# Kernel tuning notes

Hardware: AMD Instinct MI355X
Metric: run time of the kernel (lower is better)

The kernel has to match this reference:

```python
import jax, jax.numpy as jnp
import numpy as np
from jax import lax

CAP = 15.0
EPS = 1e-6

def _rmsnorm(x, w):
    xf = x.astype(jnp.float32)
    var = jnp.mean(xf * xf, axis=-1, keepdims=True)
    return w * (xf * lax.rsqrt(var + EPS)).astype(x.dtype)

def _softcap_sigmoid(x):
    return jax.nn.sigmoid(CAP * jnp.tanh(x / CAP))

def setup_inputs() -> dict:
    key = jax.random.key(0)
    ks = jax.random.split(key, 4)
    B, S, D, P = 8, 2048, 1024, 1365
    x = jax.random.normal(ks[0], (B, S, D), dtype=jnp.float32)
    h0 = jnp.zeros((B, P), dtype=jnp.float32)
    ln_weight = jnp.ones((D,), dtype=jnp.float32)
    gate_w = jax.random.normal(ks[1], (3 * P, D), dtype=jnp.float32) * 0.02
    cell_w = jax.random.normal(ks[2], (P, D), dtype=jnp.float32) * 0.02
    out_w = jax.random.normal(ks[3], (D, P), dtype=jnp.float32) * 0.02
    return {"x": x, "h0": h0, "ln_weight": ln_weight, "gate_w": gate_w,
            "cell_w": cell_w, "out_w": out_w}

def reference(x, h0, ln_weight, gate_w, cell_w, out_w):
    B, S, D = x.shape
    P = cell_w.shape[0]
    residual = x
    xn = _rmsnorm(x, ln_weight)
    # gates: [B,S,3P] -> [B,S,3,P]
    gates = jnp.einsum('bsd,gd->bsg', xn, gate_w).reshape(B, S, 3, P)
    g = _softcap_sigmoid(gates)
    i_gate, f_gate, o_gate = g[:, :, 0], g[:, :, 1], g[:, :, 2]
    c_input = jnp.einsum('bsd,pd->bsp', xn, cell_w)
    # sequential sLSTM recurrence over time via scan; xs are time-major [S,B,P]
    xs = (jnp.swapaxes(c_input, 0, 1), jnp.swapaxes(i_gate, 0, 1),
          jnp.swapaxes(f_gate, 0, 1), jnp.swapaxes(o_gate, 0, 1))
    def step(h, ts):
        c_t, i_t, f_t, o_t = ts
        h = f_t * h + i_t * jnp.tanh(c_t)
        return h, o_t * jnp.tanh(h)
    h_final, ys = lax.scan(step, h0, xs)
    output = jnp.swapaxes(ys, 0, 1)  # [B,S,P]
    out = residual + jnp.einsum('bsp,dp->bsd', output, out_w)
    return (out, h_final)
```

## Files before the change

kernel.cpp:

```cpp
#include <hip/hip_runtime.h>
#include <hip/hip_bf16.h>
#include <cstdint>

#define B_   8
#define S_   2048
#define D_   1024
#define P_   1365
#define M_   (B_*S_)
#define KP   1408
#define NGCP (4*KP)
#define CHUNK 32
#define CMAX (S_/CHUNK)

typedef __attribute__((ext_vector_type(8))) short bf16x8;
typedef __attribute__((ext_vector_type(4))) float f32x4;
typedef __attribute__((ext_vector_type(4))) unsigned short u16x4;

__device__ __forceinline__ float fast_rcp(float x) {
  return __builtin_amdgcn_rcpf(x);
}
__device__ __forceinline__ float fast_tanh(float x) {
  float e = __expf(2.0f * x);
  return 1.0f - 2.0f * fast_rcp(e + 1.0f);
}
__device__ __forceinline__ float softcap_sig(float x) {
  float u = x * (1.0f / 15.0f);
  float z = -x + x * u * u * (1.0f / 3.0f);
  return fast_rcp(1.0f + __expf(z));
}
__device__ __forceinline__ float bf2f(unsigned short u) {
  union { float f; unsigned int i; } x; x.i = ((unsigned)u) << 16; return x.f;
}
__device__ __forceinline__ unsigned short f2bf(float f) {
  __hip_bfloat16 h = __float2bfloat16(f);
  return *reinterpret_cast<unsigned short*>(&h);
}
__device__ __forceinline__ void gload_lds16(const void* g, void* l) {
  __builtin_amdgcn_global_load_lds(
      (const __attribute__((address_space(1))) uint32_t*)g,
      (__attribute__((address_space(3))) uint32_t*)l,
      16, 0, 0);
}

__global__ void k_prep_wgc(const float* __restrict__ gate_w,
                           const float* __restrict__ cell_w,
                           __hip_bfloat16* __restrict__ wgc) {
  int gid = blockIdx.x * blockDim.x + threadIdx.x;
  int idx = gid * 4;
  int r = idx >> 10, c = idx & 1023;
  int g = r / KP;
  int rr = r - g * KP;
  f32x4 v = {0.f, 0.f, 0.f, 0.f};
  if (rr < P_) {
    if (g < 3) v = __builtin_nontemporal_load((const f32x4*)(gate_w + (size_t)(g * P_ + rr) * D_ + c));
    else       v = __builtin_nontemporal_load((const f32x4*)(cell_w + (size_t)rr * D_ + c));
  }
  __hip_bfloat16* dst = wgc + idx;
  dst[0] = __float2bfloat16(v.x); dst[1] = __float2bfloat16(v.y);
  dst[2] = __float2bfloat16(v.z); dst[3] = __float2bfloat16(v.w);
}

__global__ void k_prep_wout(const float* __restrict__ out_w,
                            __hip_bfloat16* __restrict__ wout) {
  int gid = blockIdx.x * blockDim.x + threadIdx.x;
  int idx = gid * 4;
  int d = idx / KP, p = idx - d * KP;
  __hip_bfloat16* dst = wout + idx;
  #pragma unroll
  for (int j = 0; j < 4; ++j) {
    int pp = p + j;
    float v = (pp < P_) ? __builtin_nontemporal_load(out_w + (size_t)d * P_ + pp) : 0.f;
    dst[j] = __float2bfloat16(v);
  }
}

__global__ __launch_bounds__(256) void k_rmsnorm(const float* __restrict__ x,
                                                 const float* __restrict__ w,
                                                 __hip_bfloat16* __restrict__ xn) {
  __shared__ float red[4];
  int m = blockIdx.x;
  int tid = threadIdx.x;
  f32x4 v = __builtin_nontemporal_load(((const f32x4*)(x + (size_t)m * D_)) + tid);
  float ss = v.x * v.x + v.y * v.y + v.z * v.z + v.w * v.w;
  #pragma unroll
  for (int off = 32; off > 0; off >>= 1) ss += __shfl_down(ss, off);
  if ((tid & 63) == 0) red[tid >> 6] = ss;
  __syncthreads();
  float tot = red[0] + red[1] + red[2] + red[3];
  float scale = rsqrtf(tot * (1.0f / (float)D_) + 1e-6f);
  f32x4 wv = ((const f32x4*)w)[tid];
  __hip_bfloat16* o = xn + (size_t)m * D_ + tid * 4;
  o[0] = __float2bfloat16(v.x * scale * wv.x);
  o[1] = __float2bfloat16(v.y * scale * wv.y);
  o[2] = __float2bfloat16(v.z * scale * wv.z);
  o[3] = __float2bfloat16(v.w * scale * wv.w);
}

template<int LDK, int KT, bool GATES>
__global__ __launch_bounds__(512) void k_gemm256(
    const __hip_bfloat16* __restrict__ A,
    const __hip_bfloat16* __restrict__ Bw,
    __hip_bfloat16* __restrict__ pi, __hip_bfloat16* __restrict__ pf,
    __hip_bfloat16* __restrict__ po, __hip_bfloat16* __restrict__ ptc,
    const float* __restrict__ xres, float* __restrict__ out,
    int s0, int sc_shift, int NBY) {
  __shared__ __align__(16) char smem[131072];
  __hip_bfloat16* ldsA = (__hip_bfloat16*)smem;
  __hip_bfloat16* ldsB = (__hip_bfloat16*)(smem + 65536);
  const int tid = threadIdx.x;
  const int lane = tid & 63;
  const int wid = tid >> 6;
  const int wm = wid >> 2, wn = wid & 3;
  const int lr = lane & 15, lg = lane >> 4;

  const int NX = gridDim.x / NBY;
  const int cpx = gridDim.x >> 3;
  const int w2 = (blockIdx.x & 7) * cpx + (blockIdx.x >> 3);
  const int by = w2 / NX;
  const int bx = w2 - by * NX;
  const int rl0 = by * 256;
  const int col0 = bx * 256;
  const int scm = (1 << sc_shift) - 1;

  auto grow_of = [&](int rl) -> size_t {
    int bb = rl >> sc_shift;
    return (size_t)bb * S_ + s0 + (rl & scm);
  };

  auto stage_full = [&](int buf, int kt) {
    const int k0 = kt * 64;
    #pragma unroll
    for (int it = 0; it < 4; ++it) {
      int off = (it * 512 + tid) * 8;
      int r = off >> 6, c = off & 63;
      int csrc = c ^ ((r & 7) << 3);
      size_t ar = GATES ? grow_of(rl0 + r) : (size_t)(rl0 + r);
      gload_lds16(A + ar * LDK + k0 + csrc, ldsA + buf * 16384 + off);
      gload_lds16(Bw + (size_t)(col0 + r) * LDK + k0 + csrc, ldsB + buf * 16384 + off);
    }
  };

  const f32x4 zero = {0.f, 0.f, 0.f, 0.f};
  f32x4 acc[8][4];
  #pragma unroll
  for (int i = 0; i < 8; ++i)
    #pragma unroll
    for (int j = 0; j < 4; ++j) acc[i][j] = zero;

  stage_full(0, 0);
  __syncthreads();
  for (int kt = 0; kt < KT; ++kt) {
    const int cur = kt & 1;
    if (kt + 1 < KT) stage_full(cur ^ 1, kt + 1);
    #pragma unroll
    for (int ks = 0; ks < 2; ++ks) {
      bf16x8 af[8], bfr[4];
      #pragma unroll
      for (int mi = 0; mi < 8; ++mi) {
        int R = wm * 128 + mi * 16 + lr;
        int ec = (ks * 32 + lg * 8) ^ ((R & 7) << 3);
        af[mi] = *(const bf16x8*)&ldsA[cur * 16384 + R * 64 + ec];
      }
      #pragma unroll
      for (int ni = 0; ni < 4; ++ni) {
        int R = wn * 64 + ni * 16 + lr;
        int ec = (ks * 32 + lg * 8) ^ ((R & 7) << 3);
        bfr[ni] = *(const bf16x8*)&ldsB[cur * 16384 + R * 64 + ec];
      }
      #pragma unroll
      for (int mi = 0; mi < 8; ++mi)
        #pragma unroll
        for (int ni = 0; ni < 4; ++ni)
          acc[mi][ni] = __builtin_amdgcn_mfma_f32_16x16x32_bf16(af[mi], bfr[ni], acc[mi][ni], 0, 0, 0);
    }
    __syncthreads();
  }

  if (GATES) {
    __hip_bfloat16* Ct = (__hip_bfloat16*)smem;
    #pragma unroll
    for (int ni = 0; ni < 4; ++ni) {
      int cc = wn * 64 + ni * 16 + lr;
      int g = (col0 + wn * 64 + ni * 16) / KP;
      const bool istanh = (g == 3);
      #pragma unroll
      for (int mi = 0; mi < 8; ++mi) {
        #pragma unroll
        for (int j = 0; j < 4; ++j) {
          int rr = wm * 128 + mi * 16 + lg * 4 + j;
          float v = acc[mi][ni][j];
          Ct[rr * 256 + cc] = __float2bfloat16(istanh ? fast_tanh(v) : softcap_sig(v));
        }
      }
    }
    __syncthreads();
    #pragma unroll
    for (int it = 0; it < 16; ++it) {
      int idx = it * 512 + tid;
      int rr = idx >> 5;
      int ck = idx & 31;
      int gn8 = col0 + ck * 8;
      int g = gn8 / KP;
      int p = gn8 - g * KP;
      __hip_bfloat16* plane = (g == 0) ? pi : (g == 1) ? pf : (g == 2) ? po : ptc;
      size_t rl = (size_t)(rl0 + rr);
      __builtin_nontemporal_store(
          *reinterpret_cast<const f32x4*>(&Ct[rr * 256 + ck * 8]),
          reinterpret_cast<f32x4*>(&plane[rl * KP + p]));
    }
  } else {
    #pragma unroll
    for (int ni = 0; ni < 4; ++ni) {
      int gn = col0 + wn * 64 + ni * 16 + lr;
      #pragma unroll
      for (int mi = 0; mi < 8; ++mi) {
        #pragma unroll
        for (int j = 0; j < 4; ++j) {
          int rl = rl0 + wm * 128 + mi * 16 + lg * 4 + j;
          size_t o2 = grow_of(rl) * D_ + gn;
          float xr = __builtin_nontemporal_load(xres + o2);
          __builtin_nontemporal_store(xr + acc[mi][ni][j], out + o2);
        }
      }
    }
  }
}

__global__ __launch_bounds__(256) void k_scan_p1(
    const __hip_bfloat16* __restrict__ pi, const __hip_bfloat16* __restrict__ pf,
    const __hip_bfloat16* __restrict__ ptc,
    float* __restrict__ Abuf, float* __restrict__ Bbuf, int C) {
  int t = blockIdx.x * blockDim.x + threadIdx.x;
  int p4 = t % (KP / 4);
  int rest = t / (KP / 4);
  int b = rest & 7;
  int c = rest >> 3;
  int p = p4 * 4;
  size_t base = ((size_t)b * C * CHUNK + (size_t)c * CHUNK) * KP + p;
  f32x4 Aa = {1.f, 1.f, 1.f, 1.f};
  f32x4 Bc = {0.f, 0.f, 0.f, 0.f};
  #pragma unroll 8
  for (int sl = 0; sl < CHUNK; ++sl) {
    size_t idx = base + (size_t)sl * KP;
    u16x4 vf = __builtin_nontemporal_load(reinterpret_cast<const u16x4*>(pf + idx));
    u16x4 vi = __builtin_nontemporal_load(reinterpret_cast<const u16x4*>(pi + idx));
    u16x4 vt = __builtin_nontemporal_load(reinterpret_cast<const u16x4*>(ptc + idx));
    float f0 = bf2f(vf.x), f1 = bf2f(vf.y), f2 = bf2f(vf.z), f3 = bf2f(vf.w);
    Aa.x *= f0; Aa.y *= f1; Aa.z *= f2; Aa.w *= f3;
    Bc.x = f0 * Bc.x + bf2f(vi.x) * bf2f(vt.x);
    Bc.y = f1 * Bc.y + bf2f(vi.y) * bf2f(vt.y);
    Bc.z = f2 * Bc.z + bf2f(vi.z) * bf2f(vt.z);
    Bc.w = f3 * Bc.w + bf2f(vi.w) * bf2f(vt.w);
  }
  size_t o = ((size_t)c * B_ + b) * KP + p;
  *reinterpret_cast<f32x4*>(Abuf + o) = Aa;
  *reinterpret_cast<f32x4*>(Bbuf + o) = Bc;
}

__global__ __launch_bounds__(256) void k_scan_p2(
    const float* __restrict__ Abuf, const float* __restrict__ Bbuf,
    const float* __restrict__ h_in, float* __restrict__ carry,
    float* __restrict__ h_out, int C) {
  int t = blockIdx.x * blockDim.x + threadIdx.x;
  int b = t / KP;
  int p = t - b * KP;
  float h = (p < P_) ? h_in[(size_t)b * P_ + p] : 0.f;
  #pragma unroll 8
  for (int c = 0; c < C; ++c) {
    size_t o = ((size_t)c * B_ + b) * KP + p;
    carry[o] = h;
    h = Abuf[o] * h + Bbuf[o];
  }
  if (p < P_) h_out[(size_t)b * P_ + p] = h;
}

__global__ __launch_bounds__(256) void k_scan_p3(
    const __hip_bfloat16* __restrict__ pi, const __hip_bfloat16* __restrict__ pf,
    const __hip_bfloat16* __restrict__ po, __hip_bfloat16* __restrict__ ptc,
    const float* __restrict__ carry, int C) {
  int t = blockIdx.x * blockDim.x + threadIdx.x;
  int p4 = t % (KP / 4);
  int rest = t / (KP / 4);
  int b = rest & 7;
  int c = rest >> 3;
  int p = p4 * 4;
  f32x4 h4 = *reinterpret_cast<const f32x4*>(carry + ((size_t)c * B_ + b) * KP + p);
  size_t base = ((size_t)b * C * CHUNK + (size_t)c * CHUNK) * KP + p;
  #pragma unroll 4
  for (int sl = 0; sl < CHUNK; ++sl) {
    size_t idx = base + (size_t)sl * KP;
    u16x4 vf = __builtin_nontemporal_load(reinterpret_cast<const u16x4*>(pf + idx));
    u16x4 vi = __builtin_nontemporal_load(reinterpret_cast<const u16x4*>(pi + idx));
    u16x4 vo = __builtin_nontemporal_load(reinterpret_cast<const u16x4*>(po + idx));
    u16x4 vt = __builtin_nontemporal_load(reinterpret_cast<const u16x4*>(ptc + idx));
    h4.x = bf2f(vf.x) * h4.x + bf2f(vi.x) * bf2f(vt.x);
    h4.y = bf2f(vf.y) * h4.y + bf2f(vi.y) * bf2f(vt.y);
    h4.z = bf2f(vf.z) * h4.z + bf2f(vi.z) * bf2f(vt.z);
    h4.w = bf2f(vf.w) * h4.w + bf2f(vi.w) * bf2f(vt.w);
    u16x4 y;
    y.x = f2bf(bf2f(vo.x) * fast_tanh(h4.x));
    y.y = f2bf(bf2f(vo.y) * fast_tanh(h4.y));
    y.z = f2bf(bf2f(vo.z) * fast_tanh(h4.z));
    y.w = f2bf(bf2f(vo.w) * fast_tanh(h4.w));
    __builtin_nontemporal_store(y, reinterpret_cast<u16x4*>(ptc + idx));
  }
}

extern "C" void kernel_launch(void* const* d_in, const int* in_sizes, int n_in,
                              void* d_out, int out_size, void* d_ws, size_t ws_size,
                              hipStream_t stream) {
  const float* x      = (const float*)d_in[0];
  const float* h0     = (const float*)d_in[1];
  const float* lnw    = (const float*)d_in[2];
  const float* gate_w = (const float*)d_in[3];
  const float* cell_w = (const float*)d_in[4];
  const float* out_w  = (const float*)d_in[5];
  float* out  = (float*)d_out;
  float* hfin = out + (size_t)M_ * D_;

  size_t off = 0;
  char* ws = (char*)d_ws;
  __hip_bfloat16* xn   = (__hip_bfloat16*)(ws + off); off += (size_t)M_ * D_ * 2;
  __hip_bfloat16* wgc  = (__hip_bfloat16*)(ws + off); off += (size_t)NGCP * D_ * 2;
  __hip_bfloat16* wout = (__hip_bfloat16*)(ws + off); off += (size_t)D_ * KP * 2;
  float* hbuf          = (float*)(ws + off);          off += (size_t)B_ * P_ * 4;
  float* Abuf          = (float*)(ws + off);          off += (size_t)CMAX * B_ * KP * 4;
  float* Bbuf          = (float*)(ws + off);          off += (size_t)CMAX * B_ * KP * 4;
  float* carry         = (float*)(ws + off);          off += (size_t)CMAX * B_ * KP * 4;
  off = (off + 255) & ~(size_t)255;

  int nchunks = 1;
  while (nchunks < 16) {
    size_t planes = 4ull * B_ * (S_ / nchunks) * KP * 2;
    if (off + planes <= ws_size) break;
    nchunks <<= 1;
  }
  const int Sc = S_ / nchunks;
  const int C = Sc / CHUNK;
  int sc_shift = 0;
  while ((1 << sc_shift) < Sc) ++sc_shift;
  __hip_bfloat16* pi  = (__hip_bfloat16*)(ws + off); off += (size_t)B_ * Sc * KP * 2;
  __hip_bfloat16* pf  = (__hip_bfloat16*)(ws + off); off += (size_t)B_ * Sc * KP * 2;
  __hip_bfloat16* po  = (__hip_bfloat16*)(ws + off); off += (size_t)B_ * Sc * KP * 2;
  __hip_bfloat16* ptc = (__hip_bfloat16*)(ws + off); off += (size_t)B_ * Sc * KP * 2;

  k_prep_wgc<<<dim3(NGCP * D_ / 1024), dim3(256), 0, stream>>>(gate_w, cell_w, wgc);
  k_prep_wout<<<dim3(D_ * KP / 1024), dim3(256), 0, stream>>>(out_w, wout);
  k_rmsnorm<<<dim3(M_), dim3(256), 0, stream>>>(x, lnw, xn);

  for (int c = 0; c < nchunks; ++c) {
    int s0 = c * Sc;
    const int NBY = B_ * Sc / 256;
    k_gemm256<D_, D_/64, true><<<dim3((NGCP / 256) * NBY), dim3(512), 0, stream>>>(
        xn, wgc, pi, pf, po, ptc, nullptr, nullptr, s0, sc_shift, NBY);
    int np1 = B_ * C * (KP / 4);
    k_scan_p1<<<dim3(np1 / 256), dim3(256), 0, stream>>>(pi, pf, ptc, Abuf, Bbuf, C);
    k_scan_p2<<<dim3(B_ * KP / 256), dim3(256), 0, stream>>>(
        Abuf, Bbuf, (c == 0) ? h0 : hbuf, carry,
        (c == nchunks - 1) ? hfin : hbuf, C);
    k_scan_p3<<<dim3(np1 / 256), dim3(256), 0, stream>>>(pi, pf, po, ptc, carry, C);
    k_gemm256<KP, KP/64, false><<<dim3((D_ / 256) * NBY), dim3(512), 0, stream>>>(
        ptc, wout, nullptr, nullptr, nullptr, nullptr, x, out, s0, sc_shift, NBY);
  }
}
```

Baseline: 440.0 us.

## Interleave input and cell weight tiles to fuse i*tanh(c) into gate GEMM epilogue

Reorders the packed gate/cell weight matrix so that each 256-column GEMM tile holds 128 input-gate columns next to the matching 128 cell columns. The epilogue can then compute i*tanh(c) in place and write one combined plane instead of two. This removes one bf16 intermediate plane of writes and reads from the scan kernels and lowers workspace need, which may also allow fewer sequence chunks. The cost is a more complex epilogue and an extra bf16 rounding of the product.

After: 429.0 us. 1.03x faster.

```diff
diff --git a/kernel.cpp b/kernel.cpp
--- a/kernel.cpp
+++ b/kernel.cpp
@@ -48,12 +48,22 @@
   int gid = blockIdx.x * blockDim.x + threadIdx.x;
   int idx = gid * 4;
   int r = idx >> 10, c = idx & 1023;
-  int g = r / KP;
-  int rr = r - g * KP;
   f32x4 v = {0.f, 0.f, 0.f, 0.f};
-  if (rr < P_) {
-    if (g < 3) v = __builtin_nontemporal_load((const f32x4*)(gate_w + (size_t)(g * P_ + rr) * D_ + c));
-    else       v = __builtin_nontemporal_load((const f32x4*)(cell_w + (size_t)rr * D_ + c));
+  if (r < 2 * KP) {
+    int t = r >> 8, lo = r & 255;
+    if (lo < 128) {
+      int pr = t * 128 + lo;
+      if (pr < P_) v = __builtin_nontemporal_load((const f32x4*)(gate_w + (size_t)pr * D_ + c));
+    } else {
+      int pr = t * 128 + (lo - 128);
+      if (pr < P_) v = __builtin_nontemporal_load((const f32x4*)(cell_w + (size_t)pr * D_ + c));
+    }
+  } else if (r < 3 * KP) {
+    int pr = r - 2 * KP;
+    if (pr < P_) v = __builtin_nontemporal_load((const f32x4*)(gate_w + (size_t)(P_ + pr) * D_ + c));
+  } else {
+    int pr = r - 3 * KP;
+    if (pr < P_) v = __builtin_nontemporal_load((const f32x4*)(gate_w + (size_t)(2 * P_ + pr) * D_ + c));
   }
   __hip_bfloat16* dst = wgc + idx;
   dst[0] = __float2bfloat16(v.x); dst[1] = __float2bfloat16(v.y);
@@ -100,8 +110,8 @@
 __global__ __launch_bounds__(512) void k_gemm256(
     const __hip_bfloat16* __restrict__ A,
     const __hip_bfloat16* __restrict__ Bw,
-    __hip_bfloat16* __restrict__ pi, __hip_bfloat16* __restrict__ pf,
-    __hip_bfloat16* __restrict__ po, __hip_bfloat16* __restrict__ ptc,
+    __hip_bfloat16* __restrict__ pitc, __hip_bfloat16* __restrict__ pf,
+    __hip_bfloat16* __restrict__ po,
     const float* __restrict__ xres, float* __restrict__ out,
     int s0, int sc_shift, int NBY) {
   __shared__ __align__(16) char smem[131072];
@@ -178,11 +188,12 @@
 
   if (GATES) {
     __hip_bfloat16* Ct = (__hip_bfloat16*)smem;
+    const bool isIC = (col0 < 2 * KP);
     #pragma unroll
     for (int ni = 0; ni < 4; ++ni) {
-      int cc = wn * 64 + ni * 16 + lr;
-      int g = (col0 + wn * 64 + ni * 16) / KP;
-      const bool istanh = (g == 3);
+      int cbase = wn * 64 + ni * 16;
+      int cc = cbase + lr;
+      const bool istanh = isIC && (cbase >= 128);
       #pragma unroll
       for (int mi = 0; mi < 8; ++mi) {
         #pragma unroll
@@ -194,19 +205,45 @@
       }
     }
     __syncthreads();
-    #pragma unroll
-    for (int it = 0; it < 16; ++it) {
-      int idx = it * 512 + tid;
-      int rr = idx >> 5;
-      int ck = idx & 31;
-      int gn8 = col0 + ck * 8;
-      int g = gn8 / KP;
-      int p = gn8 - g * KP;
-      __hip_bfloat16* plane = (g == 0) ? pi : (g == 1) ? pf : (g == 2) ? po : ptc;
-      size_t rl = (size_t)(rl0 + rr);
-      __builtin_nontemporal_store(
-          *reinterpret_cast<const f32x4*>(&Ct[rr * 256 + ck * 8]),
-          reinterpret_cast<f32x4*>(&plane[rl * KP + p]));
+    if (isIC) {
+      const int t = col0 >> 8;
+      #pragma unroll
+      for (int it = 0; it < 8; ++it) {
+        int idx = it * 512 + tid;
+        int rr = idx >> 4;
+        int ck = idx & 15;
+        u16x4 y[2];
+        #pragma unroll
+        for (int h = 0; h < 2; ++h) {
+          #pragma unroll
+          for (int j = 0; j < 4; ++j) {
+            int cp = ck * 8 + h * 4 + j;
+            float iv = bf2f(*(const unsigned short*)&Ct[rr * 256 + cp]);
+            float cv = bf2f(*(const unsigned short*)&Ct[rr * 256 + 128 + cp]);
+            y[h][j] = f2bf(iv * cv);
+          }
+        }
+        size_t rl = (size_t)(rl0 + rr);
+        int p0 = t * 128 + ck * 8;
+        __builtin_nontemporal_store(y[0], reinterpret_cast<u16x4*>(&pitc[rl * KP + p0]));
+        __builtin_nontemporal_store(y[1], reinterpret_cast<u16x4*>(&pitc[rl * KP + p0 + 4]));
+      }
+    } else {
+      const int coff = col0 - 2 * KP;
+      #pragma unroll
+      for (int it = 0; it < 16; ++it) {
+        int idx = it * 512 + tid;
+        int rr = idx >> 5;
+        int ck = idx & 31;
+        int gn8 = coff + ck * 8;
+        int g = gn8 / KP;
+        int p = gn8 - g * KP;
+        __hip_bfloat16* plane = g ? po : pf;
+        size_t rl = (size_t)(rl0 + rr);
+        __builtin_nontemporal_store(
+            *reinterpret_cast<const f32x4*>(&Ct[rr * 256 + ck * 8]),
+            reinterpret_cast<f32x4*>(&plane[rl * KP + p]));
+      }
     }
   } else {
     #pragma unroll
@@ -227,8 +264,7 @@
 }
 
 __global__ __launch_bounds__(256) void k_scan_p1(
-    const __hip_bfloat16* __restrict__ pi, const __hip_bfloat16* __restrict__ pf,
-    const __hip_bfloat16* __restrict__ ptc,
+    const __hip_bfloat16* __restrict__ pitc, const __hip_bfloat16* __restrict__ pf,
     float* __restrict__ Abuf, float* __restrict__ Bbuf, int C) {
   int t = blockIdx.x * blockDim.x + threadIdx.x;
   int p4 = t % (KP / 4);
@@ -243,14 +279,13 @@
   for (int sl = 0; sl < CHUNK; ++sl) {
     size_t idx = base + (size_t)sl * KP;
     u16x4 vf = __builtin_nontemporal_load(reinterpret_cast<const u16x4*>(pf + idx));
-    u16x4 vi = __builtin_nontemporal_load(reinterpret_cast<const u16x4*>(pi + idx));
-    u16x4 vt = __builtin_nontemporal_load(reinterpret_cast<const u16x4*>(ptc + idx));
+    u16x4 vt = __builtin_nontemporal_load(reinterpret_cast<const u16x4*>(pitc + idx));
     float f0 = bf2f(vf.x), f1 = bf2f(vf.y), f2 = bf2f(vf.z), f3 = bf2f(vf.w);
     Aa.x *= f0; Aa.y *= f1; Aa.z *= f2; Aa.w *= f3;
-    Bc.x = f0 * Bc.x + bf2f(vi.x) * bf2f(vt.x);
-    Bc.y = f1 * Bc.y + bf2f(vi.y) * bf2f(vt.y);
-    Bc.z = f2 * Bc.z + bf2f(vi.z) * bf2f(vt.z);
-    Bc.w = f3 * Bc.w + bf2f(vi.w) * bf2f(vt.w);
+    Bc.x = f0 * Bc.x + bf2f(vt.x);
+    Bc.y = f1 * Bc.y + bf2f(vt.y);
+    Bc.z = f2 * Bc.z + bf2f(vt.z);
+    Bc.w = f3 * Bc.w + bf2f(vt.w);
   }
   size_t o = ((size_t)c * B_ + b) * KP + p;
   *reinterpret_cast<f32x4*>(Abuf + o) = Aa;
@@ -275,8 +310,8 @@
 }
 
 __global__ __launch_bounds__(256) void k_scan_p3(
-    const __hip_bfloat16* __restrict__ pi, const __hip_bfloat16* __restrict__ pf,
-    const __hip_bfloat16* __restrict__ po, __hip_bfloat16* __restrict__ ptc,
+    __hip_bfloat16* __restrict__ pitc, const __hip_bfloat16* __restrict__ pf,
+    const __hip_bfloat16* __restrict__ po,
     const float* __restrict__ carry, int C) {
   int t = blockIdx.x * blockDim.x + threadIdx.x;
   int p4 = t % (KP / 4);
@@ -290,19 +325,18 @@
   for (int sl = 0; sl < CHUNK; ++sl) {
     size_t idx = base + (size_t)sl * KP;
     u16x4 vf = __builtin_nontemporal_load(reinterpret_cast<const u16x4*>(pf + idx));
-    u16x4 vi = __builtin_nontemporal_load(reinterpret_cast<const u16x4*>(pi + idx));
     u16x4 vo = __builtin_nontemporal_load(reinterpret_cast<const u16x4*>(po + idx));
-    u16x4 vt = __builtin_nontemporal_load(reinterpret_cast<const u16x4*>(ptc + idx));
-    h4.x = bf2f(vf.x) * h4.x + bf2f(vi.x) * bf2f(vt.x);
-    h4.y = bf2f(vf.y) * h4.y + bf2f(vi.y) * bf2f(vt.y);
-    h4.z = bf2f(vf.z) * h4.z + bf2f(vi.z) * bf2f(vt.z);
-    h4.w = bf2f(vf.w) * h4.w + bf2f(vi.w) * bf2f(vt.w);
+    u16x4 vt = __builtin_nontemporal_load(reinterpret_cast<const u16x4*>(pitc + idx));
+    h4.x = bf2f(vf.x) * h4.x + bf2f(vt.x);
+    h4.y = bf2f(vf.y) * h4.y + bf2f(vt.y);
+    h4.z = bf2f(vf.z) * h4.z + bf2f(vt.z);
+    h4.w = bf2f(vf.w) * h4.w + bf2f(vt.w);
     u16x4 y;
     y.x = f2bf(bf2f(vo.x) * fast_tanh(h4.x));
     y.y = f2bf(bf2f(vo.y) * fast_tanh(h4.y));
     y.z = f2bf(bf2f(vo.z) * fast_tanh(h4.z));
     y.w = f2bf(bf2f(vo.w) * fast_tanh(h4.w));
-    __builtin_nontemporal_store(y, reinterpret_cast<u16x4*>(ptc + idx));
+    __builtin_nontemporal_store(y, reinterpret_cast<u16x4*>(pitc + idx));
   }
 }
 
@@ -331,7 +365,7 @@
 
   int nchunks = 1;
   while (nchunks < 16) {
-    size_t planes = 4ull * B_ * (S_ / nchunks) * KP * 2;
+    size_t planes = 3ull * B_ * (S_ / nchunks) * KP * 2;
     if (off + planes <= ws_size) break;
     nchunks <<= 1;
   }
@@ -339,10 +373,9 @@
   const int C = Sc / CHUNK;
   int sc_shift = 0;
   while ((1 << sc_shift) < Sc) ++sc_shift;
-  __hip_bfloat16* pi  = (__hip_bfloat16*)(ws + off); off += (size_t)B_ * Sc * KP * 2;
-  __hip_bfloat16* pf  = (__hip_bfloat16*)(ws + off); off += (size_t)B_ * Sc * KP * 2;
-  __hip_bfloat16* po  = (__hip_bfloat16*)(ws + off); off += (size_t)B_ * Sc * KP * 2;
-  __hip_bfloat16* ptc = (__hip_bfloat16*)(ws + off); off += (size_t)B_ * Sc * KP * 2;
+  __hip_bfloat16* pitc = (__hip_bfloat16*)(ws + off); off += (size_t)B_ * Sc * KP * 2;
+  __hip_bfloat16* pf   = (__hip_bfloat16*)(ws + off); off += (size_t)B_ * Sc * KP * 2;
+  __hip_bfloat16* po   = (__hip_bfloat16*)(ws + off); off += (size_t)B_ * Sc * KP * 2;
 
   k_prep_wgc<<<dim3(NGCP * D_ / 1024), dim3(256), 0, stream>>>(gate_w, cell_w, wgc);
   k_prep_wout<<<dim3(D_ * KP / 1024), dim3(256), 0, stream>>>(out_w, wout);
@@ -352,14 +385,14 @@
     int s0 = c * Sc;
     const int NBY = B_ * Sc / 256;
     k_gemm256<D_, D_/64, true><<<dim3((NGCP / 256) * NBY), dim3(512), 0, stream>>>(
-        xn, wgc, pi, pf, po, ptc, nullptr, nullptr, s0, sc_shift, NBY);
+        xn, wgc, pitc, pf, po, nullptr, nullptr, s0, sc_shift, NBY);
     int np1 = B_ * C * (KP / 4);
-    k_scan_p1<<<dim3(np1 / 256), dim3(256), 0, stream>>>(pi, pf, ptc, Abuf, Bbuf, C);
+    k_scan_p1<<<dim3(np1 / 256), dim3(256), 0, stream>>>(pitc, pf, Abuf, Bbuf, C);
     k_scan_p2<<<dim3(B_ * KP / 256), dim3(256), 0, stream>>>(
         Abuf, Bbuf, (c == 0) ? h0 : hbuf, carry,
         (c == nchunks - 1) ? hfin : hbuf, C);
-    k_scan_p3<<<dim3(np1 / 256), dim3(256), 0, stream>>>(pi, pf, po, ptc, carry, C);
+    k_scan_p3<<<dim3(np1 / 256), dim3(256), 0, stream>>>(pitc, pf, po, carry, C);
     k_gemm256<KP, KP/64, false><<<dim3((D_ / 256) * NBY), dim3(512), 0, stream>>>(
-        ptc, wout, nullptr, nullptr, nullptr, nullptr, x, out, s0, sc_shift, NBY);
-  }
-}
+        pitc, wout, nullptr, nullptr, nullptr, x, out, s0, sc_shift, NBY);
+  }
+}
```
